# Kernel optimization log

Hardware: AMD Instinct MI355X
Metric: run time of the kernel (lower is better)

Reference implementation:

```python
import jax, jax.numpy as jnp
import numpy as np

B, S, C, T = 256, 128, 64, 60
ENC, COL, RNN, ATT, ACT, TYP = 512, 512, 512, 512, 128, 64
NPROD, NTYPE = 97, 32
LS, PTEMP, CTEMP = 0.2, 1.0, 1.0
NEG = -1e9


def setup_inputs() -> dict:
    key = jax.random.key(0)
    ks = jax.random.split(key, 24)
    enc = jax.random.normal(ks[0], (B, S, ENC), jnp.float32)
    col_enc = jax.random.normal(ks[1], (B, C, COL), jnp.float32)
    enc_lens = jax.random.randint(ks[2], (B,), 1, S + 1)
    col_lens = jax.random.randint(ks[3], (B,), 1, C + 1)
    action_kind = jax.random.randint(ks[4], (B, T), 0, 3)  # 0=ApplyRule,1=Reduce,2=SelectColumn
    tgt_lens = jax.random.randint(ks[5], (B,), 1, T + 1)
    prod_ids = jax.random.randint(ks[6], (B, T), 0, NPROD)
    col_ids = jax.random.randint(ks[7], (B, T), 0, C) % col_lens[:, None]
    parent_prod = jax.random.randint(ks[8], (B, T), 0, NPROD)
    parent_type = jax.random.randint(ks[9], (B, T), 0, NTYPE)
    parent_time = jax.random.randint(ks[10], (B, T), 0, T) % jnp.maximum(jnp.arange(T), 1)[None, :]
    g = lambda k, shp: jax.random.normal(k, shp, jnp.float32) * 0.02
    IN = ACT + ATT + ACT + TYP + RNN  # a_tm1 | att_tm1 | parent_prod | parent_type | parent_h
    return dict(
        enc=enc, col_enc=col_enc, enc_lens=enc_lens, col_lens=col_lens,
        action_kind=action_kind, tgt_lens=tgt_lens, prod_ids=prod_ids,
        col_ids=col_ids, parent_prod=parent_prod, parent_type=parent_type,
        parent_time=parent_time,
        prod_embed=g(ks[11], (NPROD + 1, ACT)),
        type_embed=g(ks[12], (NTYPE, TYP)),
        b_lin=jnp.zeros((NPROD + 1,), jnp.float32),
        W_ih=g(ks[13], (IN, 4 * RNN)), W_hh=g(ks[14], (RNN, 4 * RNN)),
        b_lstm=jnp.zeros((4 * RNN,), jnp.float32),
        W_att_q=g(ks[15], (RNN, ENC)),
        W_att_vec=g(ks[16], (ENC + RNN, ATT)),
        W_r1=g(ks[17], (ATT, 4 * ATT)), b_r1=jnp.zeros((4 * ATT,), jnp.float32),
        W_r2=g(ks[18], (4 * ATT, ACT)), b_r2=jnp.zeros((ACT,), jnp.float32),
        W_col_in=g(ks[19], (COL, ACT)),
        W_ptr=g(ks[20], (ATT, COL)),
        w_mem=g(ks[21], (ATT, 1)),
    )


def reference(enc, col_enc, enc_lens, col_lens, action_kind, tgt_lens, prod_ids,
              col_ids, parent_prod, parent_type, parent_time,
              prod_embed, type_embed, b_lin, W_ih, W_hh, b_lstm,
              W_att_q, W_att_vec, W_r1, b_r1, W_r2, b_r2,
              W_col_in, W_ptr, w_mem):
    enc_mask = jnp.arange(S)[None, :] < enc_lens[:, None]   # [B,S]
    col_valid = jnp.arange(C)[None, :] < col_lens[:, None]  # [B,C]
    col_in_embed = jnp.einsum('bcd,da->bca', col_enc, W_col_in)  # column_rnn_input, [B,C,ACT]

    # previous-step actions (a_{t-1}); dummy zeros at t=0 (x is zeroed there anyway)
    shift = lambda a: jnp.concatenate([jnp.zeros_like(a[:, :1]), a[:, :-1]], axis=1)
    kind_p, pid_p, cid_p = shift(action_kind), shift(prod_ids), shift(col_ids)

    def scan_step(carry, xs):
        h, c, att, hist, appear, acc = carry
        t, kp, pp, cp, kind, pid, cid, fprod, ftype, ptime = xs
        # --- prep step input ---
        prev_valid = (t - 1) < tgt_lens
        e_rule = prod_embed[jnp.where(kp == 1, NPROD, pp)]                      # [B,ACT]
        e_col = jnp.take_along_axis(col_in_embed, cp[:, None, None], axis=1)[:, 0]
        a_embed = jnp.where((kp == 2)[:, None], e_col, e_rule)
        a_embed = jnp.where(prev_valid[:, None], a_embed, 0.0)
        parent_h = hist[ptime, jnp.arange(B)]                                   # [B,RNN]
        x = jnp.concatenate([a_embed, att, prod_embed[fprod], type_embed[ftype], parent_h], axis=-1)
        x = jnp.where(t == 0, 0.0, x)
        # --- LSTMCell (torch gate order i,f,g,o) ---
        gates = x @ W_ih + h @ W_hh + b_lstm
        i, f, g_, o = jnp.split(gates, 4, axis=-1)
        c_new = jax.nn.sigmoid(f) * c + jax.nn.sigmoid(i) * jnp.tanh(g_)
        h_new = jax.nn.sigmoid(o) * jnp.tanh(c_new)
        # --- attention over encoder ---
        scores = jnp.einsum('bd,bsd->bs', h_new @ W_att_q, enc)
        scores = jnp.where(enc_mask, scores, NEG)
        ctx = jnp.einsum('bs,bsd->bd', jax.nn.softmax(scores, axis=-1), enc)
        att_new = jnp.tanh(jnp.concatenate([ctx, h_new], axis=-1) @ W_att_vec)
        # --- production readout (tied output embedding) ---
        emb_q = jnp.tanh(att_new @ W_r1 + b_r1) @ W_r2 + b_r2
        rule_lp = jax.nn.log_softmax((emb_q @ prod_embed.T + b_lin) / PTEMP, axis=-1)
        # --- pointer net over columns with memory gate ---
        gate = jax.nn.sigmoid(att_new @ w_mem)                                  # [B,1]
        w_c = jnp.einsum('bd,bcd->bc', att_new @ W_ptr, col_enc)
        weights = w_c * appear * gate + w_c * (1.0 - appear) * (1.0 - gate)
        weights = jnp.where(col_valid, weights, NEG) / CTEMP
        col_lp = jax.nn.log_softmax(weights, axis=-1)
        # --- per-example log prob of gold action ---
        valid = t < tgt_lens
        lp_rule = jnp.take_along_axis(rule_lp, jnp.where(kind == 1, NPROD, pid)[:, None], axis=1)[:, 0]
        lp_col_raw = jnp.take_along_axis(col_lp, cid[:, None], axis=1)[:, 0]
        col_sum = jnp.sum(jnp.where(col_valid, col_lp, 0.0), axis=-1)
        lp_col = (1.0 - LS) * lp_col_raw + LS * col_sum / col_lens
        lp = jnp.where(kind == 2, lp_col, lp_rule)
        acc = acc + jnp.where(valid, lp, 0.0)
        # --- state updates (appear mask updated after use, matching torch) ---
        appear = jnp.maximum(appear, ((kind == 2) & valid)[:, None] * jax.nn.one_hot(cid, C, dtype=appear.dtype))
        hist = hist.at[t].set(h_new)
        return (h_new, c_new, att_new, hist, appear, acc), None

    carry0 = (
        jnp.zeros((B, RNN), jnp.float32), jnp.zeros((B, RNN), jnp.float32),
        jnp.zeros((B, ATT), jnp.float32), jnp.zeros((T, B, RNN), jnp.float32),
        jnp.zeros((B, C), jnp.float32), jnp.zeros((B,), jnp.float32),
    )
    xs = (jnp.arange(T), kind_p.T, pid_p.T, cid_p.T, action_kind.T, prod_ids.T,
          col_ids.T, parent_prod.T, parent_type.T, parent_time.T)
    (_, _, _, _, _, acc), _ = jax.lax.scan(scan_step, carry0, xs)
    return -jnp.mean(acc)
```

## Files before the change

### kernel.cpp

```cpp
#include <hip/hip_runtime.h>
#include <math.h>

#define NB 256
#define NS 128
#define NCOL 64
#define NT 60
#define DENC 512
#define DRNN 512
#define DATT 512
#define DACT 128
#define DTYP 64
#define DG 2048
#define NEGV (-1e9f)
#define NBH 131072
#define NROW 15360
#define RPW 512
#define NRP 2624

typedef unsigned short ushort_t;
typedef __attribute__((ext_vector_type(8))) short short8;
typedef __attribute__((ext_vector_type(4))) float f32x4;

__device__ __forceinline__ float sigf(float x) { return 1.0f / (1.0f + __expf(-x)); }
__device__ __forceinline__ float tanhfast(float x) {
  x = fminf(fmaxf(x, -15.0f), 15.0f);
  float e = __expf(-2.0f * x);
  return (1.0f - e) / (1.0f + e);
}
__device__ __forceinline__ ushort_t f2bf(float f) {
  union { float f; unsigned u; } v; v.f = f;
  unsigned r = v.u + 0x7fffu + ((v.u >> 16) & 1u);
  return (ushort_t)(r >> 16);
}
__device__ __forceinline__ float bf2f(ushort_t b) {
  union { unsigned u; float f; } v; v.u = ((unsigned)b) << 16; return v.f;
}
__device__ __forceinline__ short8 cvt8(const float* p) {
  f32x4 x = *(const f32x4*)p, y = *(const f32x4*)(p + 4);
  short8 r;
  r[0]=(short)f2bf(x[0]); r[1]=(short)f2bf(x[1]); r[2]=(short)f2bf(x[2]); r[3]=(short)f2bf(x[3]);
  r[4]=(short)f2bf(y[0]); r[5]=(short)f2bf(y[1]); r[6]=(short)f2bf(y[2]); r[7]=(short)f2bf(y[3]);
  return r;
}

__global__ __launch_bounds__(256) void zero_kernel(float* __restrict__ p, int n) {
  int i = blockIdx.x * 256 + threadIdx.x;
  if (i < n) p[i] = 0.0f;
}

__global__ __launch_bounds__(256) void cvt_bf16_kernel(const float* __restrict__ src,
    ushort_t* __restrict__ dst, int n8)
{
  int i = blockIdx.x * 256 + threadIdx.x;
  if (i < n8) *(short8*)&dst[(size_t)i * 8] = cvt8(src + (size_t)i * 8);
}

__global__ __launch_bounds__(256) void pack_w(const float* __restrict__ src,
    ushort_t* __restrict__ dst, int Ksub, int Nsub, int Ntot, int K0, int N0, int ldsrc)
{
  int idx = blockIdx.x * 256 + threadIdx.x;
  if (idx >= Ksub * Nsub) return;
  int k = idx / Nsub, n = idx - k * Nsub;
  int gk = K0 + k;
  dst[((size_t)(gk >> 3) * Ntot + (N0 + n)) * 8 + (gk & 7)] =
      f2bf(src[(size_t)k * ldsrc + n]);
}

__global__ __launch_bounds__(256) void pack_wT(const float* __restrict__ W,
    ushort_t* __restrict__ dst)
{
  int idx = blockIdx.x * 256 + threadIdx.x;
  if (idx >= 512 * 512) return;
  int r = idx >> 9, d = idx & 511;
  dst[((size_t)(d >> 3) * 512 + r) * 8 + (d & 7)] = f2bf(W[(size_t)r * 512 + d]);
}

__global__ __launch_bounds__(256) void r2p_kernel(const float* __restrict__ W_r2,
    const float* __restrict__ prod_embed, const float* __restrict__ b_r2,
    const float* __restrict__ b_lin, ushort_t* __restrict__ Wr2p,
    float* __restrict__ bias2)
{
  int idx = blockIdx.x * 256 + threadIdx.x;
  if (idx >= 2049 * 98) return;
  int k = idx / 98, j = idx - k * 98;
  const float* pe = prod_embed + (size_t)j * DACT;
  if (k < 2048) {
    const float* wr = W_r2 + (size_t)k * DACT;
    float a = 0.f;
    #pragma unroll 8
    for (int d = 0; d < DACT; ++d) a = fmaf(wr[d], pe[d], a);
    Wr2p[((size_t)(k >> 3) * 128 + j) * 8 + (k & 7)] = f2bf(a);
  } else {
    float a = b_lin[j];
    #pragma unroll 8
    for (int d = 0; d < DACT; ++d) a = fmaf(b_r2[d], pe[d], a);
    bias2[j] = a;
  }
}

__global__ __launch_bounds__(64) void appear_kernel(const int* __restrict__ action_kind,
    const int* __restrict__ tgt_lens, const int* __restrict__ col_ids,
    float* __restrict__ appear_all)
{
  int b = blockIdx.x, c = threadIdx.x;
  float ap = 0.f;
  int tl = tgt_lens[b];
  for (int t = 0; t < NT; ++t) {
    appear_all[((size_t)t * NB + b) * 64 + c] = ap;
    if (t < tl && action_kind[b * NT + t] == 2 && col_ids[b * NT + t] == c) ap = 1.f;
  }
}

__global__ __launch_bounds__(256) void gemm_bf16(
    const float* __restrict__ A1, int lda1,
    const ushort_t* __restrict__ Bp, ushort_t* __restrict__ Cb, int ldc,
    int N, int K)
{
  __shared__ short As[2][4096];
  __shared__ short Bs[2][4096];
  const int tid = threadIdx.x;
  const int lane = tid & 63, w = tid >> 6;
  const int wr = w >> 1, wc = w & 1;
  const int mBase = blockIdx.y * 64, nBase = blockIdx.x * 64;
  const int nt = K >> 6;
  f32x4 ra0[2], ra1[2];
  short8 rb[2];
  auto issue = [&](int kt) {
    #pragma unroll
    for (int s = 0; s < 2; ++s) {
      int slot = tid + s * 256;
      int kc = slot >> 6, m = slot & 63;
      int k0 = (kt << 6) + kc * 8;
      const float* p = A1 + (size_t)(mBase + m) * lda1 + k0;
      ra0[s] = *(const f32x4*)p;
      ra1[s] = *(const f32x4*)(p + 4);
      rb[s] = *(const short8*)(Bp + ((size_t)(k0 >> 3) * N + nBase + m) * 8);
    }
  };
  auto store = [&](int buf) {
    #pragma unroll
    for (int s = 0; s < 2; ++s) {
      int slot = tid + s * 256;
      short8 av;
      av[0]=(short)f2bf(ra0[s][0]); av[1]=(short)f2bf(ra0[s][1]);
      av[2]=(short)f2bf(ra0[s][2]); av[3]=(short)f2bf(ra0[s][3]);
      av[4]=(short)f2bf(ra1[s][0]); av[5]=(short)f2bf(ra1[s][1]);
      av[6]=(short)f2bf(ra1[s][2]); av[7]=(short)f2bf(ra1[s][3]);
      *(short8*)&As[buf][slot * 8] = av;
      *(short8*)&Bs[buf][slot * 8] = rb[s];
    }
  };
  f32x4 z4 = {0.f,0.f,0.f,0.f};
  f32x4 acc[2][2] = {{z4,z4},{z4,z4}};
  issue(0); store(0);
  __syncthreads();
  int cur = 0;
  for (int kt = 0; kt < nt; ++kt) {
    bool more = (kt + 1 < nt);
    if (more) issue(kt + 1);
    #pragma unroll
    for (int kk = 0; kk < 2; ++kk) {
      int ko = kk * 4 + (lane >> 4);
      short8 af[2], bfr[2];
      #pragma unroll
      for (int f = 0; f < 2; ++f) {
        int row = wr * 32 + f * 16 + (lane & 15);
        af[f] = *(const short8*)&As[cur][(ko * 64 + row) * 8];
        int col = wc * 32 + f * 16 + (lane & 15);
        bfr[f] = *(const short8*)&Bs[cur][(ko * 64 + col) * 8];
      }
      #pragma unroll
      for (int i = 0; i < 2; ++i)
        #pragma unroll
        for (int j = 0; j < 2; ++j)
          acc[i][j] = __builtin_amdgcn_mfma_f32_16x16x32_bf16(af[i], bfr[j], acc[i][j], 0, 0, 0);
    }
    if (more) store(cur ^ 1);
    __syncthreads();
    cur ^= 1;
  }
  #pragma unroll
  for (int i = 0; i < 2; ++i)
    #pragma unroll
    for (int j = 0; j < 2; ++j)
      #pragma unroll
      for (int r = 0; r < 4; ++r) {
        int row = mBase + wr * 32 + i * 16 + (lane >> 4) * 4 + r;
        int col = nBase + wc * 32 + j * 16 + (lane & 15);
        Cb[(size_t)row * ldc + col] = f2bf(acc[i][j][r]);
      }
}

__global__ __launch_bounds__(256) void gemm_encwq(
    const float* __restrict__ enc, const ushort_t* __restrict__ WqTp,
    ushort_t* __restrict__ encWq, ushort_t* __restrict__ enc_b)
{
  __shared__ short Asm[32768];
  const int tid = threadIdx.x;
  const int lane = tid & 63, w = tid >> 6;
  const int wr = w >> 1, wc = w & 1;
  const int mBase = blockIdx.x * 64;
  #pragma unroll
  for (int it = 0; it < 16; ++it) {
    int o = tid + it * 256;
    int row = o >> 6, c = o & 63;
    short8 v = cvt8(enc + (size_t)(mBase + row) * 512 + c * 8);
    *(short8*)&Asm[row * 512 + ((c ^ (row & 7)) * 8)] = v;
    *(short8*)(enc_b + (size_t)(mBase + row) * 512 + c * 8) = v;
  }
  __syncthreads();
  for (int nt = 0; nt < 8; ++nt) {
    f32x4 z4 = {0.f,0.f,0.f,0.f};
    f32x4 acc[2][2] = {{z4,z4},{z4,z4}};
    short8 bb[2][4];
    auto loadBf = [&](int kt, short8* dst) {
      #pragma unroll
      for (int kk = 0; kk < 2; ++kk)
        #pragma unroll
        for (int f = 0; f < 2; ++f) {
          int ko = kt * 8 + kk * 4 + (lane >> 4);
          int col = nt * 64 + wc * 32 + f * 16 + (lane & 15);
          dst[kk * 2 + f] = *(const short8*)(WqTp + ((size_t)ko * 512 + col) * 8);
        }
    };
    loadBf(0, bb[0]);
    loadBf(1, bb[1]);
    #pragma unroll
    for (int kt = 0; kt < 8; ++kt) {
      short8 cur[4];
      #pragma unroll
      for (int i = 0; i < 4; ++i) cur[i] = bb[kt & 1][i];
      if (kt + 2 < 8) loadBf(kt + 2, bb[kt & 1]);
      #pragma unroll
      for (int kk = 0; kk < 2; ++kk) {
        int ko = kt * 8 + kk * 4 + (lane >> 4);
        short8 af[2];
        #pragma unroll
        for (int f = 0; f < 2; ++f) {
          int row = wr * 32 + f * 16 + (lane & 15);
          af[f] = *(const short8*)&Asm[row * 512 + ((ko ^ (row & 7)) * 8)];
        }
        #pragma unroll
        for (int i = 0; i < 2; ++i)
          #pragma unroll
          for (int j = 0; j < 2; ++j)
            acc[i][j] = __builtin_amdgcn_mfma_f32_16x16x32_bf16(af[i], cur[kk * 2 + j], acc[i][j], 0, 0, 0);
      }
    }
    #pragma unroll
    for (int i = 0; i < 2; ++i)
      #pragma unroll
      for (int j = 0; j < 2; ++j)
        #pragma unroll
        for (int r = 0; r < 4; ++r) {
          int row = mBase + wr * 32 + i * 16 + (lane >> 4) * 4 + r;
          int col = nt * 64 + wc * 32 + j * 16 + (lane & 15);
          encWq[(size_t)row * 512 + col] = f2bf(acc[i][j][r]);
        }
  }
}

template <class FA, class FB, class FE>
__device__ __forceinline__ void gemm_core(char* smem, FA loadA, FB loadB,
    int ktBeg, int ktEnd, FE epi)
{
  short* As = (short*)smem;
  short* Bs = (short*)smem + 8192;
  const int tid = threadIdx.x;
  const int lane = tid & 63, w = tid >> 6;
  const int wr = w >> 1, wc = w & 1;
  f32x4 z4 = {0.f,0.f,0.f,0.f};
  f32x4 acc[2][2] = {{z4,z4},{z4,z4}};
  short8 pa[2], pb[2];
  auto issue = [&](int kt) {
    #pragma unroll
    for (int s = 0; s < 2; ++s) {
      int slot = tid + s * 256;
      int kc = slot >> 6;
      int k = (kt << 6) + (kc << 3);
      pa[s] = loadA(k);
      pb[s] = loadB(slot & 63, k);
    }
  };
  auto store = [&](int buf) {
    #pragma unroll
    for (int s = 0; s < 2; ++s) {
      int slot = tid + s * 256;
      *(short8*)&As[buf * 4096 + slot * 8] = pa[s];
      *(short8*)&Bs[buf * 4096 + slot * 8] = pb[s];
    }
  };
  issue(ktBeg); store(0);
  __syncthreads();
  int cur = 0;
  for (int kt = ktBeg; kt < ktEnd; ++kt) {
    bool more = (kt + 1 < ktEnd);
    if (more) issue(kt + 1);
    #pragma unroll
    for (int kk = 0; kk < 2; ++kk) {
      int ko = kk * 4 + (lane >> 4);
      short8 af[2], bfr[2];
      #pragma unroll
      for (int f = 0; f < 2; ++f) {
        int row = wr * 32 + f * 16 + (lane & 15);
        af[f] = *(const short8*)&As[cur * 4096 + (ko * 64 + row) * 8];
        int col = wc * 32 + f * 16 + (lane & 15);
        bfr[f] = *(const short8*)&Bs[cur * 4096 + (ko * 64 + col) * 8];
      }
      #pragma unroll
      for (int i = 0; i < 2; ++i)
        #pragma unroll
        for (int j = 0; j < 2; ++j)
          acc[i][j] = __builtin_amdgcn_mfma_f32_16x16x32_bf16(af[i], bfr[j], acc[i][j], 0, 0, 0);
    }
    if (more) store(cur ^ 1);
    __syncthreads();
    cur ^= 1;
  }
  #pragma unroll
  for (int i = 0; i < 2; ++i)
    #pragma unroll
    for (int j = 0; j < 2; ++j)
      #pragma unroll
      for (int r = 0; r < 4; ++r) {
        int rl = wr * 32 + i * 16 + (lane >> 4) * 4 + r;
        int cl = wc * 32 + j * 16 + (lane & 15);
        epi(rl, cl, acc[i][j][r]);
      }
}

__global__ __launch_bounds__(256) void k1_gates(
    const int* __restrict__ action_kind, const int* __restrict__ tgt_lens,
    const int* __restrict__ prod_ids, const int* __restrict__ col_ids,
    const int* __restrict__ parent_prod, const int* __restrict__ parent_type,
    const int* __restrict__ parent_time,
    const float* __restrict__ prod_embed, const float* __restrict__ type_embed,
    const ushort_t* __restrict__ WpG, const ushort_t* __restrict__ colin_b,
    const ushort_t* __restrict__ att_all, const ushort_t* __restrict__ hist_u,
    float* __restrict__ gates0, float* __restrict__ gates1,
    float* __restrict__ gates2, float* __restrict__ gates3, int t)
{
  __shared__ __align__(16) char smem[32768];
  const int tid = threadIdx.x;
  const int nb = blockIdx.x, mb = blockIdx.y, ks = blockIdx.z;
  const int mBase = mb * 64, nBase = nb * 64;
  const int b = mBase + (tid & 63);
  int kp = action_kind[b * NT + t - 1];
  int pp = prod_ids[b * NT + t - 1];
  int cp = col_ids[b * NT + t - 1];
  bool pv = (t - 1) < tgt_lens[b];
  int fp = parent_prod[b * NT + t];
  int ft = parent_type[b * NT + t];
  int ptm = parent_time[b * NT + t];
  const ushort_t* hist_prev = hist_u + (size_t)(t - 1) * NBH;
  const ushort_t* att_prev = att_all + (size_t)(t - 1) * NB * DATT;
  auto loadA = [&](int k) -> short8 {
    short8 z = {0,0,0,0,0,0,0,0};
    if (k < 128) {
      if (!pv) return z;
      if (kp == 2) return *(const short8*)(colin_b + ((size_t)(b * NCOL + cp) * DACT + k));
      int row = (kp == 1) ? 97 : pp;
      return cvt8(prod_embed + (size_t)row * DACT + k);
    } else if (k < 640) {
      return *(const short8*)(att_prev + (size_t)b * DATT + (k - 128));
    } else if (k < 768) {
      return cvt8(prod_embed + (size_t)fp * DACT + (k - 640));
    } else if (k < 832) {
      return cvt8(type_embed + (size_t)ft * DTYP + (k - 768));
    } else if (k < 1344) {
      return *(const short8*)(hist_u + (size_t)ptm * NBH + (size_t)b * DRNN + (k - 832));
    } else {
      return *(const short8*)(hist_prev + (size_t)b * DRNN + (k - 1344));
    }
  };
  auto loadB = [&](int n, int k) -> short8 {
    return *(const short8*)(WpG + ((size_t)(k >> 3) * DG + nBase + n) * 8);
  };
  float* gp = (ks == 0) ? gates0 : (ks == 1) ? gates1 : (ks == 2) ? gates2 : gates3;
  auto epi = [&](int rl, int cl, float v) {
    gp[(size_t)(mBase + rl) * DG + nBase + cl] = v;
  };
  const int kb0 = (ks == 0) ? 0 : (ks == 1) ? 8 : (ks == 2) ? 15 : 22;
  const int kb1 = (ks == 0) ? 8 : (ks == 1) ? 15 : (ks == 2) ? 22 : 29;
  gemm_core(smem, loadA, loadB, kb0, kb1, epi);
}

struct SmemK23 { float hq[DRNN]; float ml[4][2]; float cs[4][DENC]; };
__global__ __launch_bounds__(256) void k23_lstm_attn(
    const float* __restrict__ g0, const float* __restrict__ g1,
    const float* __restrict__ g2, const float* __restrict__ g3,
    const float* __restrict__ b_lstm, float* __restrict__ cst,
    ushort_t* __restrict__ hist_t,
    const ushort_t* __restrict__ encWq, const ushort_t* __restrict__ enc_b,
    const int* __restrict__ enc_lens, ushort_t* __restrict__ ctxb)
{
  __shared__ __align__(16) SmemK23 s;
  int b = blockIdx.x, tid = threadIdx.x;
  const float* p0 = g0 + (size_t)b * DG;
  const float* p1 = g1 + (size_t)b * DG;
  const float* p2 = g2 + (size_t)b * DG;
  const float* p3 = g3 + (size_t)b * DG;
  #pragma unroll
  for (int r = 0; r < 2; ++r) {
    int j = tid + r * 256;
    float gi = p0[j] + p1[j] + p2[j] + p3[j] + b_lstm[j];
    float gf = p0[512+j] + p1[512+j] + p2[512+j] + p3[512+j] + b_lstm[512+j];
    float gg = p0[1024+j] + p1[1024+j] + p2[1024+j] + p3[1024+j] + b_lstm[1024+j];
    float go = p0[1536+j] + p1[1536+j] + p2[1536+j] + p3[1536+j] + b_lstm[1536+j];
    size_t ix = (size_t)b * DRNN + j;
    float cn = sigf(gf) * cst[ix] + sigf(gi) * tanhfast(gg);
    float hn = sigf(go) * tanhfast(cn);
    cst[ix] = cn;
    hist_t[ix] = f2bf(hn);
    s.hq[j] = hn;
  }
  __syncthreads();
  int w = tid >> 6, lane = tid & 63;
  int el = enc_lens[b];
  float q[8];
  #pragma unroll
  for (int j = 0; j < 8; ++j) q[j] = s.hq[lane * 8 + j];
  float m = -1e30f, lr = 0.f;
  float cacc[8];
  #pragma unroll
  for (int j = 0; j < 8; ++j) cacc[j] = 0.f;
  const ushort_t* eWb = encWq + (size_t)b * NS * DENC + lane * 8;
  const ushort_t* eb = enc_b + (size_t)b * NS * DENC + lane * 8;
  for (int sI = w; sI < el; sI += 4) {
    short8 xr = *(const short8*)(eWb + (size_t)sI * DENC);
    short8 er = *(const short8*)(eb + (size_t)sI * DENC);
    float d = 0.f;
    #pragma unroll
    for (int j = 0; j < 8; ++j) d = fmaf(bf2f((ushort_t)xr[j]), q[j], d);
    #pragma unroll
    for (int off = 32; off > 0; off >>= 1) d += __shfl_xor(d, off);
    float mn = fmaxf(m, d);
    float rr = __expf(m - mn), p = __expf(d - mn);
    lr = lr * rr + p;
    #pragma unroll
    for (int j = 0; j < 8; ++j) cacc[j] = cacc[j] * rr + p * bf2f((ushort_t)er[j]);
    m = mn;
  }
  if (lane == 0) { s.ml[w][0] = m; s.ml[w][1] = lr; }
  #pragma unroll
  for (int j = 0; j < 8; ++j) s.cs[w][lane * 8 + j] = cacc[j];
  __syncthreads();
  float M = fmaxf(fmaxf(s.ml[0][0], s.ml[1][0]), fmaxf(s.ml[2][0], s.ml[3][0]));
  float f0 = __expf(s.ml[0][0] - M), f1 = __expf(s.ml[1][0] - M);
  float f2 = __expf(s.ml[2][0] - M), f3 = __expf(s.ml[3][0] - M);
  float invL = 1.f / (f0 * s.ml[0][1] + f1 * s.ml[1][1] + f2 * s.ml[2][1] + f3 * s.ml[3][1]);
  #pragma unroll
  for (int rep = 0; rep < 2; ++rep) {
    int d = tid + rep * 256;
    ctxb[(size_t)b * DENC + d] =
        f2bf((f0 * s.cs[0][d] + f1 * s.cs[1][d] + f2 * s.cs[2][d] + f3 * s.cs[3][d]) * invL);
  }
}

__global__ __launch_bounds__(256) void k4_attvec(const ushort_t* __restrict__ ctxb,
    const ushort_t* __restrict__ hist_t, const ushort_t* __restrict__ WpV,
    ushort_t* __restrict__ att_all, int t)
{
  __shared__ __align__(16) char smem[32768];
  const int tid = threadIdx.x;
  const int mBase = blockIdx.y * 64, nBase = blockIdx.x * 64;
  const int b = mBase + (tid & 63);
  auto loadA = [&](int k) -> short8 {
    if (k < 512) return *(const short8*)(ctxb + (size_t)b * DENC + k);
    return *(const short8*)(hist_t + (size_t)b * DRNN + (k - 512));
  };
  auto loadB = [&](int n, int k) -> short8 {
    return *(const short8*)(WpV + ((size_t)(k >> 3) * 512 + nBase + n) * 8);
  };
  auto epi = [&](int rl, int cl, float v) {
    att_all[((size_t)t * NB + mBase + rl) * DATT + nBase + cl] = f2bf(tanhfast(v));
  };
  gemm_core(smem, loadA, loadB, 0, 16, epi);
}

__global__ __launch_bounds__(256) void kbig_r1ptr(const ushort_t* __restrict__ att_all,
    const ushort_t* __restrict__ WpRP, const float* __restrict__ b_r1,
    ushort_t* __restrict__ r1c, ushort_t* __restrict__ ptrq_all,
    float* __restrict__ gate_all, int rowBase)
{
  __shared__ __align__(16) char smem[32768];
  const int tid = threadIdx.x;
  const int bid = blockIdx.x;
  const int x = bid & 7, j = bid >> 3;
  const int mb = x * 15 + j / 41;
  const int nb = j % 41;
  const int mBase = mb * 64, nBase = nb * 64;
  const size_t grow = (size_t)rowBase + mBase + (tid & 63);
  auto loadA = [&](int k) -> short8 {
    return *(const short8*)(att_all + grow * DATT + k);
  };
  auto loadB = [&](int n, int k) -> short8 {
    return *(const short8*)(WpRP + ((size_t)(k >> 3) * NRP + nBase + n) * 8);
  };
  auto epi = [&](int rl, int cl, float v) {
    int col = nBase + cl;
    size_t gr = (size_t)rowBase + mBase + rl;
    if (col < 2048)      r1c[(size_t)(mBase + rl) * DG + col] = f2bf(tanhfast(v + b_r1[col]));
    else if (col < 2560) ptrq_all[((size_t)(gr & 255) * NT + (gr >> 8)) * RPW + (col - 2048)] = f2bf(v);
    else if (col == 2560) gate_all[gr] = v;
  };
  gemm_core(smem, loadA, loadB, 0, 8, epi);
}

__global__ __launch_bounds__(256) void klogits(const ushort_t* __restrict__ r1c,
    const ushort_t* __restrict__ Wr2p, float* __restrict__ logits_all, int rowBase)
{
  __shared__ __align__(16) char smem[32768];
  const int tid = threadIdx.x;
  const int bid = blockIdx.x;
  const int x = bid & 7, j = bid >> 3;
  const int mb = x * 15 + (j >> 1);
  const int nb = j & 1;
  const int mBase = mb * 64, nBase = nb * 64;
  auto loadA = [&](int k) -> short8 {
    return *(const short8*)(r1c + (size_t)(mBase + (tid & 63)) * DG + k);
  };
  auto loadB = [&](int n, int k) -> short8 {
    return *(const short8*)(Wr2p + ((size_t)(k >> 3) * 128 + nBase + n) * 8);
  };
  auto epi = [&](int rl, int cl, float v) {
    logits_all[((size_t)rowBase + mBase + rl) * 128 + nBase + cl] = v;
  };
  gemm_core(smem, loadA, loadB, 0, 32, epi);
}

__global__ __launch_bounds__(256) void kwc(const ushort_t* __restrict__ ptrq_all,
    const ushort_t* __restrict__ colenc_b, float* __restrict__ w_c_all)
{
  __shared__ __align__(16) char smem[32768];
  const int tid = threadIdx.x;
  const int b = blockIdx.x;
  const int tt = tid & 63;
  auto loadA = [&](int k) -> short8 {
    short8 z = {0,0,0,0,0,0,0,0};
    if (tt >= NT) return z;
    return *(const short8*)(ptrq_all + ((size_t)b * NT + tt) * RPW + k);
  };
  auto loadB = [&](int n, int k) -> short8 {
    return *(const short8*)(colenc_b + ((size_t)b * NCOL + n) * 512 + k);
  };
  auto epi = [&](int rl, int cl, float v) {
    if (rl < NT) w_c_all[((size_t)rl * NB + b) * 64 + cl] = v;
  };
  gemm_core(smem, loadA, loadB, 0, 8, epi);
}

__global__ __launch_bounds__(64) void kfinal(
    const float* __restrict__ logits_all, const float* __restrict__ bias2,
    const float* __restrict__ w_c_all, const float* __restrict__ gate_all,
    const float* __restrict__ appear_all, const int* __restrict__ col_lens,
    const int* __restrict__ tgt_lens, const int* __restrict__ action_kind,
    const int* __restrict__ prod_ids, const int* __restrict__ col_ids,
    float* __restrict__ loss_tb)
{
  int row = blockIdx.x;
  int t = row >> 8, b = row & 255;
  int c = threadIdx.x;
  float l0 = logits_all[(size_t)row * 128 + c] + bias2[c];
  float l1 = (c + 64 < 98) ? logits_all[(size_t)row * 128 + 64 + c] + bias2[64 + c] : -1e30f;
  float m = fmaxf(l0, l1);
  #pragma unroll
  for (int off = 32; off > 0; off >>= 1) m = fmaxf(m, __shfl_down(m, off));
  m = __shfl(m, 0);
  float sv = __expf(l0 - m) + ((c + 64 < 98) ? __expf(l1 - m) : 0.f);
  #pragma unroll
  for (int off = 32; off > 0; off >>= 1) sv += __shfl_down(sv, off);
  sv = __shfl(sv, 0);
  float lseR = m + __logf(sv);
  int clen = col_lens[b];
  float gate = sigf(gate_all[row]);
  float ap = appear_all[(size_t)row * 64 + c];
  float wc = w_c_all[(size_t)row * 64 + c];
  float wv = wc * (ap * gate + (1.f - ap) * (1.f - gate));
  wv = (c < clen) ? wv : NEGV;
  float m2 = wv;
  #pragma unroll
  for (int off = 32; off > 0; off >>= 1) m2 = fmaxf(m2, __shfl_down(m2, off));
  m2 = __shfl(m2, 0);
  float s2 = __expf(wv - m2);
  #pragma unroll
  for (int off = 32; off > 0; off >>= 1) s2 += __shfl_down(s2, off);
  s2 = __shfl(s2, 0);
  float lse2 = m2 + __logf(s2);
  float csum = (c < clen) ? (wv - lse2) : 0.f;
  #pragma unroll
  for (int off = 32; off > 0; off >>= 1) csum += __shfl_down(csum, off);
  int kind = action_kind[b * NT + t];
  int cid = col_ids[b * NT + t];
  float wcid = __shfl(wv, cid);
  if (c == 0) {
    int pid = prod_ids[b * NT + t];
    bool valid = t < tgt_lens[b];
    int gj = (kind == 1) ? 97 : pid;
    float lgj = logits_all[(size_t)row * 128 + gj] + bias2[gj];
    float lp_rule = lgj - lseR;
    float lp_col = 0.8f * (wcid - lse2) + 0.2f * csum / (float)clen;
    float lp = (kind == 2) ? lp_col : lp_rule;
    loss_tb[row] = valid ? lp : 0.f;
  }
}

__global__ __launch_bounds__(256) void loss_reduce(const float* __restrict__ loss_tb,
                                                   float* __restrict__ out) {
  int tid = threadIdx.x;
  float v = 0.f;
  for (int k = 0; k < NT; ++k) v += loss_tb[(size_t)k * NB + tid];
  #pragma unroll
  for (int off = 32; off > 0; off >>= 1) v += __shfl_down(v, off);
  __shared__ float part[4];
  if ((tid & 63) == 0) part[tid >> 6] = v;
  __syncthreads();
  if (tid == 0) out[0] = -(part[0] + part[1] + part[2] + part[3]) * (1.0f / NB);
}

extern "C" void kernel_launch(void* const* d_in, const int* in_sizes, int n_in,
                              void* d_out, int out_size, void* d_ws, size_t ws_size,
                              hipStream_t stream) {
  const float* enc         = (const float*)d_in[0];
  const float* col_enc     = (const float*)d_in[1];
  const int*   enc_lens    = (const int*)d_in[2];
  const int*   col_lens    = (const int*)d_in[3];
  const int*   action_kind = (const int*)d_in[4];
  const int*   tgt_lens    = (const int*)d_in[5];
  const int*   prod_ids    = (const int*)d_in[6];
  const int*   col_ids     = (const int*)d_in[7];
  const int*   parent_prod = (const int*)d_in[8];
  const int*   parent_type = (const int*)d_in[9];
  const int*   parent_time = (const int*)d_in[10];
  const float* prod_embed  = (const float*)d_in[11];
  const float* type_embed  = (const float*)d_in[12];
  const float* b_lin       = (const float*)d_in[13];
  const float* W_ih        = (const float*)d_in[14];
  const float* W_hh        = (const float*)d_in[15];
  const float* b_lstm      = (const float*)d_in[16];
  const float* W_att_q     = (const float*)d_in[17];
  const float* W_att_vec   = (const float*)d_in[18];
  const float* W_r1        = (const float*)d_in[19];
  const float* b_r1        = (const float*)d_in[20];
  const float* W_r2        = (const float*)d_in[21];
  const float* b_r2        = (const float*)d_in[22];
  const float* W_col_in    = (const float*)d_in[23];
  const float* W_ptr       = (const float*)d_in[24];
  const float* w_mem       = (const float*)d_in[25];

  float* base = (float*)d_ws;
  size_t o = 0;
  float* cst    = base + o; o += 131072;
  float* gates0 = base + o; o += 524288;
  float* gates1 = base + o; o += 524288;
  float* gates2 = base + o; o += 524288;
  float* gates3 = base + o; o += 524288;
  int zeroN = (int)o;
  ushort_t* hist_u = (ushort_t*)(base + o); o += 3932160;
  float* logits_all = (float*)hist_u;
  ushort_t* colin_b = (ushort_t*)(base + o); o += 1048576;
  float* encWq_f    = base + o; o += 8388608;
  ushort_t* encWq   = (ushort_t*)encWq_f;
  ushort_t* r1c     = (ushort_t*)encWq_f;
  float* encb_f     = base + o; o += 4194304;
  ushort_t* enc_b   = (ushort_t*)encb_f;
  ushort_t* colenc_b = (ushort_t*)encb_f;
  ushort_t* att_all  = (ushort_t*)(base + o); o += 3932160;
  ushort_t* ptrq_all = (ushort_t*)(base + o); o += 3932160;
  ushort_t* ctxb     = ptrq_all;
  float* gate_all    = base + o; o += 15360;
  float* w_c_all     = base + o; o += 983040;
  float* appear_all  = base + o; o += 983040;
  float* loss_tb     = base + o; o += 15360;
  ushort_t* WpG   = (ushort_t*)(base + o); o += 1900544;
  ushort_t* WqTp  = (ushort_t*)(base + o); o += 131072;
  ushort_t* WpV   = (ushort_t*)(base + o); o += 262144;
  ushort_t* WpRP  = (ushort_t*)(base + o); o += 671744;
  ushort_t* WpCI  = (ushort_t*)(base + o); o += 32768;
  ushort_t* Wr2p  = (ushort_t*)(base + o); o += 131072;
  float* bias2    = base + o; o += 128;
  (void)ws_size; (void)in_sizes; (void)n_in; (void)out_size;

  zero_kernel<<<(zeroN + 255) / 256, 256, 0, stream>>>(base, zeroN);
  zero_kernel<<<(671744 + 255) / 256, 256, 0, stream>>>((float*)WpRP, 671744);
  zero_kernel<<<(131072 + 255) / 256, 256, 0, stream>>>((float*)Wr2p, 131072);

  pack_w<<<(1344 * 2048 + 255) / 256, 256, 0, stream>>>(W_ih, WpG, 1344, 2048, 2048, 0, 0, 2048);
  pack_w<<<(512 * 2048 + 255) / 256, 256, 0, stream>>>(W_hh, WpG, 512, 2048, 2048, 1344, 0, 2048);
  pack_wT<<<(512 * 512 + 255) / 256, 256, 0, stream>>>(W_att_q, WqTp);
  pack_w<<<(1024 * 512 + 255) / 256, 256, 0, stream>>>(W_att_vec, WpV, 1024, 512, 512, 0, 0, 512);
  pack_w<<<(512 * 2048 + 255) / 256, 256, 0, stream>>>(W_r1, WpRP, 512, 2048, NRP, 0, 0, 2048);
  pack_w<<<(512 * 512 + 255) / 256, 256, 0, stream>>>(W_ptr, WpRP, 512, 512, NRP, 0, 2048, 512);
  pack_w<<<(512 + 255) / 256, 256, 0, stream>>>(w_mem, WpRP, 512, 1, NRP, 0, 2560, 1);
  pack_w<<<(512 * 128 + 255) / 256, 256, 0, stream>>>(W_col_in, WpCI, 512, 128, 128, 0, 0, 128);
  r2p_kernel<<<(2049 * 98 + 255) / 256, 256, 0, stream>>>(W_r2, prod_embed, b_r2, b_lin, Wr2p, bias2);
  appear_kernel<<<NB, 64, 0, stream>>>(action_kind, tgt_lens, col_ids, appear_all);

  gemm_bf16<<<dim3(2, 256), 256, 0, stream>>>(col_enc, 512, WpCI, colin_b, 128, 128, 512);
  gemm_encwq<<<512, 256, 0, stream>>>(enc, WqTp, encWq, enc_b);

  for (int t = 0; t < NT; ++t) {
    ushort_t* hist_t = hist_u + (size_t)t * NBH;
    if (t > 0)
      k1_gates<<<dim3(32, 4, 4), 256, 0, stream>>>(
          action_kind, tgt_lens, prod_ids, col_ids, parent_prod, parent_type,
          parent_time, prod_embed, type_embed, WpG, colin_b, att_all, hist_u,
          gates0, gates1, gates2, gates3, t);
    k23_lstm_attn<<<NB, 256, 0, stream>>>(gates0, gates1, gates2, gates3,
        b_lstm, cst, hist_t, encWq, enc_b, enc_lens, ctxb);
    k4_attvec<<<dim3(8, 4), 256, 0, stream>>>(ctxb, hist_t, WpV, att_all, t);
  }

  cvt_bf16_kernel<<<(1048576 + 255) / 256, 256, 0, stream>>>(col_enc, colenc_b, 1048576);
  for (int ch = 0; ch < 2; ++ch) {
    int rowBase = ch * 7680;
    kbig_r1ptr<<<4920, 256, 0, stream>>>(att_all, WpRP, b_r1, r1c,
                                         ptrq_all, gate_all, rowBase);
    klogits<<<240, 256, 0, stream>>>(r1c, Wr2p, logits_all, rowBase);
  }
  kwc<<<NB, 256, 0, stream>>>(ptrq_all, colenc_b, w_c_all);
  kfinal<<<NROW, 64, 0, stream>>>(logits_all, bias2, w_c_all, gate_all,
      appear_all, col_lens, tgt_lens, action_kind, prod_ids, col_ids, loss_tb);
  loss_reduce<<<1, 256, 0, stream>>>(loss_tb, (float*)d_out);
}
```

Measured before the change: 3.072 ms.

## Widen r1/ptr GEMM tiles to 64x128 with register-prefetched double buffering

```diff
diff --git a/kernel.cpp b/kernel.cpp
--- a/kernel.cpp
+++ b/kernel.cpp
@@ -15,7 +15,7 @@
 #define NBH 131072
 #define NROW 15360
 #define RPW 512
-#define NRP 2624
+#define NRP 2688
 
 typedef unsigned short ushort_t;
 typedef __attribute__((ext_vector_type(8))) short short8;
@@ -342,7 +342,11 @@
 {
   __shared__ __align__(16) char smem[32768];
   const int tid = threadIdx.x;
-  const int nb = blockIdx.x, mb = blockIdx.y, ks = blockIdx.z;
+  const int bid = blockIdx.x;
+  const int x = bid & 7, j = bid >> 3;
+  const int mb = x >> 1;
+  const int ks = j >> 4;
+  const int nb = ((x & 1) << 4) | (j & 15);
   const int mBase = mb * 64, nBase = nb * 64;
   const int b = mBase + (tid & 63);
   int kp = action_kind[b * NT + t - 1];
@@ -483,28 +487,91 @@
     ushort_t* __restrict__ r1c, ushort_t* __restrict__ ptrq_all,
     float* __restrict__ gate_all, int rowBase)
 {
-  __shared__ __align__(16) char smem[32768];
+  __shared__ short As[2][4096];
+  __shared__ short Bs[2][8192];
   const int tid = threadIdx.x;
+  const int lane = tid & 63, w = tid >> 6;
+  const int wr = w >> 1, wc = w & 1;
   const int bid = blockIdx.x;
   const int x = bid & 7, j = bid >> 3;
-  const int mb = x * 15 + j / 41;
-  const int nb = j % 41;
-  const int mBase = mb * 64, nBase = nb * 64;
-  const size_t grow = (size_t)rowBase + mBase + (tid & 63);
-  auto loadA = [&](int k) -> short8 {
-    return *(const short8*)(att_all + grow * DATT + k);
-  };
-  auto loadB = [&](int n, int k) -> short8 {
-    return *(const short8*)(WpRP + ((size_t)(k >> 3) * NRP + nBase + n) * 8);
-  };
-  auto epi = [&](int rl, int cl, float v) {
-    int col = nBase + cl;
-    size_t gr = (size_t)rowBase + mBase + rl;
-    if (col < 2048)      r1c[(size_t)(mBase + rl) * DG + col] = f2bf(tanhfast(v + b_r1[col]));
-    else if (col < 2560) ptrq_all[((size_t)(gr & 255) * NT + (gr >> 8)) * RPW + (col - 2048)] = f2bf(v);
-    else if (col == 2560) gate_all[gr] = v;
-  };
-  gemm_core(smem, loadA, loadB, 0, 8, epi);
+  const int mb = x * 15 + j / 21;
+  const int ng = j % 21;
+  const int mBase = mb * 64, nBase = ng * 128;
+  short8 pa[2], pb[4];
+  auto issue = [&](int kt) {
+    #pragma unroll
+    for (int s = 0; s < 2; ++s) {
+      int slot = tid + s * 256;
+      int kc = slot >> 6, m = slot & 63;
+      int k = (kt << 6) + (kc << 3);
+      pa[s] = *(const short8*)(att_all + ((size_t)rowBase + mBase + m) * DATT + k);
+    }
+    #pragma unroll
+    for (int s = 0; s < 4; ++s) {
+      int slot = tid + s * 256;
+      int kc = slot >> 7, n = slot & 127;
+      int k = (kt << 6) + (kc << 3);
+      pb[s] = *(const short8*)(WpRP + ((size_t)(k >> 3) * NRP + nBase + n) * 8);
+    }
+  };
+  auto store = [&](int buf) {
+    #pragma unroll
+    for (int s = 0; s < 2; ++s) {
+      int slot = tid + s * 256;
+      *(short8*)&As[buf][slot * 8] = pa[s];
+    }
+    #pragma unroll
+    for (int s = 0; s < 4; ++s) {
+      int slot = tid + s * 256;
+      *(short8*)&Bs[buf][slot * 8] = pb[s];
+    }
+  };
+  f32x4 z4 = {0.f,0.f,0.f,0.f};
+  f32x4 acc[2][4] = {{z4,z4,z4,z4},{z4,z4,z4,z4}};
+  issue(0); store(0);
+  __syncthreads();
+  int cur = 0;
+  for (int kt = 0; kt < 8; ++kt) {
+    bool more = (kt + 1 < 8);
+    if (more) issue(kt + 1);
+    #pragma unroll
+    for (int kk = 0; kk < 2; ++kk) {
+      int ko = kk * 4 + (lane >> 4);
+      short8 af[2], bfr[4];
+      #pragma unroll
+      for (int f = 0; f < 2; ++f) {
+        int row = wr * 32 + f * 16 + (lane & 15);
+        af[f] = *(const short8*)&As[cur][(ko * 64 + row) * 8];
+      }
+      #pragma unroll
+      for (int f = 0; f < 4; ++f) {
+        int col = wc * 64 + f * 16 + (lane & 15);
+        bfr[f] = *(const short8*)&Bs[cur][(ko * 128 + col) * 8];
+      }
+      #pragma unroll
+      for (int i = 0; i < 2; ++i)
+        #pragma unroll
+        for (int jf = 0; jf < 4; ++jf)
+          acc[i][jf] = __builtin_amdgcn_mfma_f32_16x16x32_bf16(af[i], bfr[jf], acc[i][jf], 0, 0, 0);
+    }
+    if (more) store(cur ^ 1);
+    __syncthreads();
+    cur ^= 1;
+  }
+  #pragma unroll
+  for (int i = 0; i < 2; ++i)
+    #pragma unroll
+    for (int jf = 0; jf < 4; ++jf)
+      #pragma unroll
+      for (int r = 0; r < 4; ++r) {
+        int rl = wr * 32 + i * 16 + (lane >> 4) * 4 + r;
+        int col = nBase + wc * 64 + jf * 16 + (lane & 15);
+        size_t gr = (size_t)rowBase + mBase + rl;
+        float v = acc[i][jf][r];
+        if (col < 2048)      r1c[(size_t)(mBase + rl) * DG + col] = f2bf(tanhfast(v + b_r1[col]));
+        else if (col < 2560) ptrq_all[((size_t)(gr & 255) * NT + (gr >> 8)) * RPW + (col - 2048)] = f2bf(v);
+        else if (col == 2560) gate_all[gr] = v;
+      }
 }
 
 __global__ __launch_bounds__(256) void klogits(const ushort_t* __restrict__ r1c,
@@ -675,14 +742,14 @@
   ushort_t* WpG   = (ushort_t*)(base + o); o += 1900544;
   ushort_t* WqTp  = (ushort_t*)(base + o); o += 131072;
   ushort_t* WpV   = (ushort_t*)(base + o); o += 262144;
-  ushort_t* WpRP  = (ushort_t*)(base + o); o += 671744;
+  ushort_t* WpRP  = (ushort_t*)(base + o); o += 688128;
   ushort_t* WpCI  = (ushort_t*)(base + o); o += 32768;
   ushort_t* Wr2p  = (ushort_t*)(base + o); o += 131072;
   float* bias2    = base + o; o += 128;
   (void)ws_size; (void)in_sizes; (void)n_in; (void)out_size;
 
   zero_kernel<<<(zeroN + 255) / 256, 256, 0, stream>>>(base, zeroN);
-  zero_kernel<<<(671744 + 255) / 256, 256, 0, stream>>>((float*)WpRP, 671744);
+  zero_kernel<<<(688128 + 255) / 256, 256, 0, stream>>>((float*)WpRP, 688128);
   zero_kernel<<<(131072 + 255) / 256, 256, 0, stream>>>((float*)Wr2p, 131072);
 
   pack_w<<<(1344 * 2048 + 255) / 256, 256, 0, stream>>>(W_ih, WpG, 1344, 2048, 2048, 0, 0, 2048);
@@ -702,7 +769,7 @@
   for (int t = 0; t < NT; ++t) {
     ushort_t* hist_t = hist_u + (size_t)t * NBH;
     if (t > 0)
-      k1_gates<<<dim3(32, 4, 4), 256, 0, stream>>>(
+      k1_gates<<<512, 256, 0, stream>>>(
           action_kind, tgt_lens, prod_ids, col_ids, parent_prod, parent_type,
           parent_time, prod_embed, type_embed, WpG, colin_b, att_all, hist_u,
           gates0, gates1, gates2, gates3, t);
@@ -714,7 +781,7 @@
   cvt_bf16_kernel<<<(1048576 + 255) / 256, 256, 0, stream>>>(col_enc, colenc_b, 1048576);
   for (int ch = 0; ch < 2; ++ch) {
     int rowBase = ch * 7680;
-    kbig_r1ptr<<<4920, 256, 0, stream>>>(att_all, WpRP, b_r1, r1c,
+    kbig_r1ptr<<<2520, 256, 0, stream>>>(att_all, WpRP, b_r1, r1c,
                                          ptrq_all, gate_all, rowBase);
     klogits<<<240, 256, 0, stream>>>(r1c, Wr2p, logits_all, rowBase);
   }
```

Measured after the change: 3.065 ms. About the same (-0.2%).
